# Performance work log

Measured on AMD Instinct MI355X. Metric: run time of the kernel, lower is better.

Reference implementation:

```python
import jax, jax.numpy as jnp
import numpy as np

C_IN, C_P1, C_G1, N_OUT = 512, 256, 256, 6
B, H, W = 256, 19, 19


def mish(x):
    return x * jnp.tanh(jax.nn.softplus(x))


def setup_inputs() -> dict:
    key = jax.random.key(0)
    ks = jax.random.split(key, 8)
    x = jax.random.normal(ks[0], (B, C_IN, H, W), dtype=jnp.float32)
    mask = jnp.ones((B, 1, H, W), dtype=jnp.float32)
    conv1p_w = jax.random.normal(ks[1], (C_P1, C_IN), dtype=jnp.float32) * (1.0 / np.sqrt(C_IN))
    conv1g_w = jax.random.normal(ks[2], (C_G1, C_IN), dtype=jnp.float32) * (1.0 / np.sqrt(C_IN))
    beta_g = jnp.zeros((C_G1,), dtype=jnp.float32)
    linear_g_w = jax.random.normal(ks[3], (C_P1, 3 * C_G1), dtype=jnp.float32) * (1.0 / np.sqrt(3 * C_G1))
    beta2 = jnp.zeros((C_P1,), dtype=jnp.float32)
    conv2p_w = jax.random.normal(ks[4], (N_OUT, C_P1), dtype=jnp.float32) * (0.3 / np.sqrt(C_P1))
    return {"x": x, "mask": mask, "conv1p_w": conv1p_w, "conv1g_w": conv1g_w,
            "beta_g": beta_g, "linear_g_w": linear_g_w, "beta2": beta2, "conv2p_w": conv2p_w}


def reference(x, mask, conv1p_w, conv1g_w, beta_g, linear_g_w, beta2, conv2p_w):
    # 1x1 convs are channel GEMMs
    outp = jnp.einsum('bchw,oc->bohw', x, conv1p_w)              # [B, C_P1, H, W]
    outg = jnp.einsum('bchw,oc->bohw', x, conv1g_w)              # [B, C_G1, H, W]
    # BiasMask (scale=None) + Mish
    outg = mish((outg + beta_g[None, :, None, None]) * mask)
    # KataGPool: mean, scaled mean, max (masked)
    mask_sum_hw = jnp.sum(mask, axis=(2, 3), keepdims=True)      # [B,1,1,1]
    layer_mean = jnp.sum(outg * mask, axis=(2, 3), keepdims=True) / mask_sum_hw
    layer_max = jnp.max(outg + (mask - 1.0), axis=(2, 3), keepdims=True)
    sqrt_off = (jnp.sqrt(mask_sum_hw) - 14.0) / 10.0
    pooled = jnp.concatenate([layer_mean, layer_mean * sqrt_off, layer_max], axis=1)  # [B, 3*C_G1, 1, 1]
    pooled = pooled[:, :, 0, 0]                                  # [B, 3*C_G1]
    g = pooled @ linear_g_w.T                                    # [B, C_P1]
    # broadcast-add, BiasMask, Mish
    outp = mish((outp + g[:, :, None, None] + beta2[None, :, None, None]) * mask)
    # final 1x1 conv + invalid-move penalty
    outp = jnp.einsum('bchw,oc->bohw', outp, conv2p_w)           # [B, 6, H, W]
    outp = outp - (1.0 - mask) * 5000.0
    return outp.reshape(outp.shape[0], outp.shape[1], -1)        # [B, 6, H*W]
```

## Files before the change

### kernel.cpp

```cpp
#include <hip/hip_runtime.h>
#include <math.h>

#define BATCH 256
#define CIN   512
#define CP    256
#define HW    361
#define NOUT  6

typedef short bf16x8 __attribute__((ext_vector_type(8)));
typedef float f32x4  __attribute__((ext_vector_type(4)));

__device__ __forceinline__ short f2bf(float f) {
    unsigned u = __float_as_uint(f);
    u += 0x7fffu + ((u >> 16) & 1u);
    return (short)(u >> 16);
}
__device__ __forceinline__ float bf2f(short s) {
    return __uint_as_float(((unsigned)(unsigned short)s) << 16);
}
__device__ __forceinline__ float mish_f(float v) {
    float u = __expf(v);
    float a = 1.f + u;
    float w = a * a;
    float r = v * (w - 1.f) * __builtin_amdgcn_rcpf(w + 1.f);
    return (v > 30.f) ? v : r;
}
__device__ __forceinline__ void gl_lds16(const void* g, void* l) {
    __builtin_amdgcn_global_load_lds(
        (const __attribute__((address_space(1))) void*)g,
        (__attribute__((address_space(3))) void*)l, 16, 0, 0);
}

__global__ __launch_bounds__(256) void k0_weights(
    const float* __restrict__ w1p, const float* __restrict__ w1g,
    short* __restrict__ wT)
{
    int g = blockIdx.x * 256 + threadIdx.x;
    int half = g >> 14;
    int kb   = (g >> 10) & 15;
    int row  = (g >> 2) & 255;
    int s    = g & 3;
    int sc   = s ^ ((row >> 1) & 3);
    const float* src = (half == 0) ? (w1p + (size_t)row * CIN)
                                   : (w1g + (size_t)row * CIN);
    int c = kb * 32 + sc * 8;
    float f[8];
    *(float4*)(f)     = *(const float4*)(src + c);
    *(float4*)(f + 4) = *(const float4*)(src + c + 4);
    bf16x8 v;
    #pragma unroll
    for (int i = 0; i < 8; ++i) v[i] = f2bf(f[i]);
    *(bf16x8*)((char*)wT + (size_t)half * 262144 + kb * 16384 + row * 64 + s * 16) = v;
}

__global__ __launch_bounds__(512, 4) void k1_conv1(
    const float* __restrict__ x, const short* __restrict__ wT,
    const float* __restrict__ mask, const float* __restrict__ beta_g,
    short* __restrict__ outp_pre, float* __restrict__ psum, float* __restrict__ pmax)
{
    int orig = blockIdx.x;
    int newid = (orig & 7) * 192 + (orig >> 3);
    int half = newid & 1;
    int nb = newid >> 1;
    int n = nb % 3;
    int b = nb / 3;

    const int tid = threadIdx.x;
    const int lane = tid & 63, wid = tid >> 6;
    const int wm = wid >> 1, wn = wid & 1;
    const int lc = lane & 15, lg = lane >> 4;
    const int hw0 = n * 128;

    __shared__ __align__(16) short As[3][8192];
    __shared__ __align__(16) short Bs[3][4096];
    __shared__ float maskS[128], betaS[256];
    float* redS = (float*)(&As[0][0]);
    float* redM = redS + 512;

    if (tid < 128) {
        int hwg_ = hw0 + tid;
        maskS[tid] = (hwg_ < HW) ? mask[b * HW + hwg_] : 0.f;
    }
    if (tid < 256) betaS[tid] = beta_g[tid];
    asm volatile("s_waitcnt vmcnt(0) lgkmcnt(0)" ::: "memory");
    __builtin_amdgcn_sched_barrier(0);

    const int brow = tid & 127;
    const int bs   = tid >> 7;
    const int hwg  = hw0 + brow;
    const bool bvalid = hwg < HW;
    const float* xb = x + ((size_t)b * CIN + bs * 8) * HW + hwg;
    const int bDstOff = brow * 64 + ((bs ^ ((brow >> 1) & 3)) * 16);
    char* bDstBase = (char*)Bs;

    const char* aSrc = (const char*)wT + (size_t)half * 262144 + tid * 16;
    char* aDst = (char*)As + tid * 16;

    int aOff[4], bOff[4];
    #pragma unroll
    for (int mf = 0; mf < 4; ++mf) {
        int r = wm * 64 + mf * 16 + lc;
        aOff[mf] = r * 64 + ((lg ^ ((r >> 1) & 3)) * 16);
    }
    #pragma unroll
    for (int nf = 0; nf < 4; ++nf) {
        int r = wn * 64 + nf * 16 + lc;
        bOff[nf] = r * 64 + ((lg ^ ((r >> 1) & 3)) * 16);
    }

    float regB[8];
    #pragma unroll
    for (int i = 0; i < 8; ++i) regB[i] = 0.f;

    f32x4 acc[4][4];
    #pragma unroll
    for (int i = 0; i < 4; ++i)
        #pragma unroll
        for (int j = 0; j < 4; ++j)
            acc[i][j] = (f32x4){0.f, 0.f, 0.f, 0.f};

#define BLOAD(kb)                                                          \
    do {                                                                   \
        const float* src_ = xb + (size_t)(kb) * 32 * HW;                   \
        _Pragma("unroll")                                                  \
        for (int i_ = 0; i_ < 8; ++i_) {                                   \
            regB[i_] = bvalid ? src_[(size_t)i_ * HW] : 0.f;               \
        }                                                                  \
    } while (0)

#define BWRITE(buf)                                                        \
    do {                                                                   \
        bf16x8 o_;                                                         \
        _Pragma("unroll")                                                  \
        for (int i_ = 0; i_ < 8; ++i_) o_[i_] = f2bf(regB[i_]);            \
        *(bf16x8*)(bDstBase + (buf) * 8192 + bDstOff) = o_;                \
    } while (0)

#define ALOAD(buf, kb)                                                     \
    do {                                                                   \
        gl_lds16(aSrc + (kb) * 16384,        aDst + (buf) * 16384);        \
        gl_lds16(aSrc + (kb) * 16384 + 8192, aDst + (buf) * 16384 + 8192); \
    } while (0)

    ALOAD(0, 0); BLOAD(0);
    ALOAD(1, 1);
    asm volatile("s_waitcnt vmcnt(2)" ::: "memory");
    __builtin_amdgcn_sched_barrier(0);
    BWRITE(0);
    BLOAD(1);
    asm volatile("s_waitcnt lgkmcnt(0)" ::: "memory");
    __builtin_amdgcn_s_barrier();
    __builtin_amdgcn_sched_barrier(0);

    #pragma unroll
    for (int t = 0; t < 16; ++t) {
        const int buf = t % 3;
        const char* ab = (const char*)As + buf * 16384;
        const char* bb = (const char*)Bs + buf * 8192;

        bf16x8 aF[4], bF[4];
        #pragma unroll
        for (int mf = 0; mf < 4; ++mf) aF[mf] = *(const bf16x8*)(ab + aOff[mf]);
        #pragma unroll
        for (int nf = 0; nf < 4; ++nf) bF[nf] = *(const bf16x8*)(bb + bOff[nf]);

        if (t < 14) { ALOAD((t + 2) % 3, t + 2); }

        __builtin_amdgcn_s_setprio(1);
        #pragma unroll
        for (int mf = 0; mf < 4; ++mf)
            #pragma unroll
            for (int nf = 0; nf < 4; ++nf)
                acc[mf][nf] = __builtin_amdgcn_mfma_f32_16x16x32_bf16(
                    aF[mf], bF[nf], acc[mf][nf], 0, 0, 0);
        __builtin_amdgcn_s_setprio(0);

        if (t < 14) {
            asm volatile("s_waitcnt vmcnt(2)" ::: "memory");
            __builtin_amdgcn_sched_barrier(0);
            BWRITE((t + 1) % 3);
            BLOAD(t + 2);
        } else if (t == 14) {
            asm volatile("s_waitcnt vmcnt(0)" ::: "memory");
            __builtin_amdgcn_sched_barrier(0);
            BWRITE(15 % 3);
        }
        if (t < 15) {
            asm volatile("s_waitcnt lgkmcnt(0)" ::: "memory");
            __builtin_amdgcn_s_barrier();
            __builtin_amdgcn_sched_barrier(0);
        }
    }
    __syncthreads();

    if (half == 0) {
        #pragma unroll
        for (int mf = 0; mf < 4; ++mf) {
            int ch = wm * 64 + mf * 16 + lg * 4;
            #pragma unroll
            for (int nf = 0; nf < 4; ++nf) {
                int hw = hw0 + wn * 64 + nf * 16 + lc;
                if (hw < HW) {
                    #pragma unroll
                    for (int j = 0; j < 4; ++j)
                        outp_pre[((size_t)(b * CP + ch + j)) * HW + hw] = f2bf(acc[mf][nf][j]);
                }
            }
        }
    } else {
        #pragma unroll
        for (int mf = 0; mf < 4; ++mf) {
            #pragma unroll
            for (int j = 0; j < 4; ++j) {
                int rloc = wm * 64 + mf * 16 + lg * 4 + j;
                float beta = betaS[rloc];
                float s = 0.f, mx = -INFINITY;
                #pragma unroll
                for (int nf = 0; nf < 4; ++nf) {
                    int cl = wn * 64 + nf * 16 + lc;
                    int hw = hw0 + cl;
                    float mv = maskS[cl];
                    float val = mish_f((acc[mf][nf][j] + beta) * mv);
                    if (hw < HW) {
                        s += val * mv;
                        mx = fmaxf(mx, val + mv - 1.f);
                    }
                }
                #pragma unroll
                for (int off = 1; off < 16; off <<= 1) {
                    s += __shfl_xor(s, off, 64);
                    mx = fmaxf(mx, __shfl_xor(mx, off, 64));
                }
                if (lc == 0) { redS[rloc * 2 + wn] = s; redM[rloc * 2 + wn] = mx; }
            }
        }
        __syncthreads();
        if (tid < 256) {
            float s = redS[tid * 2] + redS[tid * 2 + 1];
            float mx = fmaxf(redM[tid * 2], redM[tid * 2 + 1]);
            psum[((size_t)(b * CP + tid)) * 3 + n] = s;
            pmax[((size_t)(b * CP + tid)) * 3 + n] = mx;
        }
    }
#undef BLOAD
#undef BWRITE
#undef ALOAD
}

__global__ __launch_bounds__(256) void k2_pool_linear(
    const float* __restrict__ mask, const float* __restrict__ psum,
    const float* __restrict__ pmax, const float* __restrict__ lw,
    float* __restrict__ g_out)
{
    int b = blockIdx.x, t = threadIdx.x;
    __shared__ float pooled[768];
    __shared__ float msr[4];

    float s = 0.f;
    for (int i = t; i < HW; i += 256) s += mask[b * HW + i];
    #pragma unroll
    for (int off = 1; off < 64; off <<= 1) s += __shfl_xor(s, off, 64);
    if ((t & 63) == 0) msr[t >> 6] = s;
    __syncthreads();
    float msum = msr[0] + msr[1] + msr[2] + msr[3];

    {
        int c = t;
        const float* ps = psum + (size_t)(b * CP + c) * 3;
        const float* pm = pmax + (size_t)(b * CP + c) * 3;
        float s3 = ps[0] + ps[1] + ps[2];
        float m3 = fmaxf(fmaxf(pm[0], pm[1]), pm[2]);
        float mean = s3 / msum;
        float sq = (sqrtf(msum) - 14.f) * 0.1f;
        pooled[c] = mean; pooled[256 + c] = mean * sq; pooled[512 + c] = m3;
    }
    __syncthreads();
    {
        int o = t;
        const float4* wrow = (const float4*)(lw + (size_t)o * 768);
        float acc = 0.f;
        #pragma unroll 8
        for (int j = 0; j < 192; ++j) {
            float4 w4 = wrow[j];
            float4 p4 = *(const float4*)&pooled[j * 4];
            acc += p4.x * w4.x + p4.y * w4.y + p4.z * w4.z + p4.w * w4.w;
        }
        g_out[b * CP + o] = acc;
    }
}

__global__ __launch_bounds__(256) void k3_final(
    const short* __restrict__ outp_pre, const float* __restrict__ mask,
    const float* __restrict__ g_out, const float* __restrict__ beta2,
    const float* __restrict__ w2, float* __restrict__ out)
{
    int ht = blockIdx.x, b = blockIdx.y;
    int t = threadIdx.x;
    __shared__ float w2S[NOUT * 256];
    __shared__ float gbS[256];
    __shared__ float part[NOUT][256];

    for (int i = t; i < NOUT * 256; i += 256) w2S[i] = w2[i];
    gbS[t] = g_out[b * CP + t] + beta2[t];
    __syncthreads();

    int hw = t & 63, cg = t >> 6;
    int hwg = ht * 64 + hw;
    bool valid = hwg < HW;
    float maskv = valid ? mask[b * HW + hwg] : 0.f;

    float acc[NOUT] = {0.f, 0.f, 0.f, 0.f, 0.f, 0.f};
    const short* src = outp_pre + ((size_t)(b * CP + cg * 64)) * HW + hwg;
    #pragma unroll 4
    for (int ci = 0; ci < 64; ++ci) {
        float v = valid ? bf2f(src[(size_t)ci * HW]) : 0.f;
        float mm = mish_f((v + gbS[cg * 64 + ci]) * maskv);
        #pragma unroll
        for (int o = 0; o < NOUT; ++o) acc[o] += mm * w2S[o * 256 + cg * 64 + ci];
    }
    #pragma unroll
    for (int o = 0; o < NOUT; ++o) part[o][t] = acc[o];
    __syncthreads();

    for (int idx = t; idx < NOUT * 64; idx += 256) {
        int o = idx >> 6, h2 = idx & 63;
        int hg = ht * 64 + h2;
        if (hg < HW) {
            float mv = mask[b * HW + hg];
            float sum = part[o][h2] + part[o][64 + h2] + part[o][128 + h2] + part[o][192 + h2];
            out[((size_t)(b * NOUT + o)) * HW + hg] = sum - (1.f - mv) * 5000.f;
        }
    }
}

extern "C" void kernel_launch(void* const* d_in, const int* in_sizes, int n_in,
                              void* d_out, int out_size, void* d_ws, size_t ws_size,
                              hipStream_t stream) {
    const float* x     = (const float*)d_in[0];
    const float* mask  = (const float*)d_in[1];
    const float* w1p   = (const float*)d_in[2];
    const float* w1g   = (const float*)d_in[3];
    const float* betag = (const float*)d_in[4];
    const float* lw    = (const float*)d_in[5];
    const float* beta2 = (const float*)d_in[6];
    const float* w2    = (const float*)d_in[7];
    float* out = (float*)d_out;

    char* ws = (char*)d_ws;
    short* outp_pre = (short*)(ws);
    short* wT       = (short*)(ws + 47316992);
    float* psum     = (float*)(ws + 47841280);
    float* pmax     = (float*)(ws + 48627712);
    float* g_out    = (float*)(ws + 49414144);

    hipLaunchKernelGGL(k0_weights, dim3(128), dim3(256), 0, stream, w1p, w1g, wT);
    hipLaunchKernelGGL(k1_conv1, dim3(1536), dim3(512), 0, stream,
                       x, wT, mask, betag, outp_pre, psum, pmax);
    hipLaunchKernelGGL(k2_pool_linear, dim3(BATCH), dim3(256), 0, stream,
                       mask, psum, pmax, lw, g_out);
    hipLaunchKernelGGL(k3_final, dim3(6, BATCH), dim3(256), 0, stream,
                       outp_pre, mask, g_out, beta2, w2, out);
    (void)in_sizes; (void)n_in; (void)out_size; (void)ws_size;
}
```

Measured before the change: 142.9 us.

## Restructure conv1 tiles: full 512-channel M per block, whole-K x tile in LDS

Each block now computes all 512 output channels (both conv branches) for 64 spatial positions instead of one 256-channel half for 128 positions. The x tile for the block's full K extent is kept resident in LDS, so each x element is read from global memory once per block rather than once per half. The weight tile is no longer staged through LDS; MFMA A-fragments load directly from the global (cached) transposed weights. This drops the triple-buffered pipeline and most barriers, but puts weight fetches on the MFMA critical path, uses 64 KB of LDS per block, and doubles the number of pooling partials that k2 must reduce.

After: 161.2 us. +12.8%, slower.

```diff
diff --git a/kernel.cpp b/kernel.cpp
--- a/kernel.cpp
+++ b/kernel.cpp
@@ -6,6 +6,7 @@
 #define CP    256
 #define HW    361
 #define NOUT  6
+#define NT    6
 
 typedef short bf16x8 __attribute__((ext_vector_type(8)));
 typedef float f32x4  __attribute__((ext_vector_type(4)));
@@ -25,32 +26,25 @@
     float r = v * (w - 1.f) * __builtin_amdgcn_rcpf(w + 1.f);
     return (v > 30.f) ? v : r;
 }
-__device__ __forceinline__ void gl_lds16(const void* g, void* l) {
-    __builtin_amdgcn_global_load_lds(
-        (const __attribute__((address_space(1))) void*)g,
-        (__attribute__((address_space(3))) void*)l, 16, 0, 0);
-}
 
 __global__ __launch_bounds__(256) void k0_weights(
     const float* __restrict__ w1p, const float* __restrict__ w1g,
     short* __restrict__ wT)
 {
     int g = blockIdx.x * 256 + threadIdx.x;
-    int half = g >> 14;
-    int kb   = (g >> 10) & 15;
-    int row  = (g >> 2) & 255;
-    int s    = g & 3;
-    int sc   = s ^ ((row >> 1) & 3);
-    const float* src = (half == 0) ? (w1p + (size_t)row * CIN)
-                                   : (w1g + (size_t)row * CIN);
-    int c = kb * 32 + sc * 8;
+    int kb  = g >> 11;
+    int row = (g >> 2) & 511;
+    int s   = g & 3;
+    const float* src = (row < 256) ? (w1p + (size_t)row * CIN)
+                                   : (w1g + (size_t)(row - 256) * CIN);
+    int c = kb * 32 + s * 8;
     float f[8];
     *(float4*)(f)     = *(const float4*)(src + c);
     *(float4*)(f + 4) = *(const float4*)(src + c + 4);
     bf16x8 v;
     #pragma unroll
     for (int i = 0; i < 8; ++i) v[i] = f2bf(f[i]);
-    *(bf16x8*)((char*)wT + (size_t)half * 262144 + kb * 16384 + row * 64 + s * 16) = v;
+    *(bf16x8*)((char*)wT + (size_t)kb * 32768 + row * 64 + s * 16) = v;
 }
 
 __global__ __launch_bounds__(512, 4) void k1_conv1(
@@ -60,57 +54,55 @@
 {
     int orig = blockIdx.x;
     int newid = (orig & 7) * 192 + (orig >> 3);
-    int half = newid & 1;
-    int nb = newid >> 1;
-    int n = nb % 3;
-    int b = nb / 3;
+    int n = newid % NT;
+    int b = newid / NT;
 
     const int tid = threadIdx.x;
     const int lane = tid & 63, wid = tid >> 6;
-    const int wm = wid >> 1, wn = wid & 1;
     const int lc = lane & 15, lg = lane >> 4;
-    const int hw0 = n * 128;
-
-    __shared__ __align__(16) short As[3][8192];
-    __shared__ __align__(16) short Bs[3][4096];
-    __shared__ float maskS[128], betaS[256];
-    float* redS = (float*)(&As[0][0]);
-    float* redM = redS + 512;
-
-    if (tid < 128) {
+    const int hw0 = n * 64;
+
+    __shared__ __align__(16) short Bs[64 * 512];
+    __shared__ float maskS[64];
+    __shared__ float betaS[256];
+
+    if (tid < 64) {
         int hwg_ = hw0 + tid;
         maskS[tid] = (hwg_ < HW) ? mask[b * HW + hwg_] : 0.f;
     }
     if (tid < 256) betaS[tid] = beta_g[tid];
-    asm volatile("s_waitcnt vmcnt(0) lgkmcnt(0)" ::: "memory");
-    __builtin_amdgcn_sched_barrier(0);
-
-    const int brow = tid & 127;
-    const int bs   = tid >> 7;
+
+    const int brow = tid & 63;
+    const int bgrp = tid >> 6;
     const int hwg  = hw0 + brow;
     const bool bvalid = hwg < HW;
-    const float* xb = x + ((size_t)b * CIN + bs * 8) * HW + hwg;
-    const int bDstOff = brow * 64 + ((bs ^ ((brow >> 1) & 3)) * 16);
-    char* bDstBase = (char*)Bs;
-
-    const char* aSrc = (const char*)wT + (size_t)half * 262144 + tid * 16;
-    char* aDst = (char*)As + tid * 16;
-
-    int aOff[4], bOff[4];
-    #pragma unroll
-    for (int mf = 0; mf < 4; ++mf) {
-        int r = wm * 64 + mf * 16 + lc;
-        aOff[mf] = r * 64 + ((lg ^ ((r >> 1) & 3)) * 16);
-    }
+    const float* xb = x + (size_t)b * CIN * HW + hwg;
+
+#define BFILL(s_)                                                           \
+    do {                                                                    \
+        int s__ = (s_);                                                     \
+        const float* fsrc_ = xb + (size_t)(s__ * 8) * HW;                   \
+        bf16x8 o_;                                                          \
+        _Pragma("unroll")                                                   \
+        for (int i_ = 0; i_ < 8; ++i_)                                      \
+            o_[i_] = f2bf(bvalid ? fsrc_[(size_t)i_ * HW] : 0.f);           \
+        *(bf16x8*)((char*)Bs + brow * 1024 + ((s__ ^ (brow & 7)) * 16)) = o_; \
+    } while (0)
+
+    BFILL(bgrp);
+    BFILL(bgrp + 8);
+    BFILL(bgrp + 16);
+    BFILL(bgrp + 24);
+    __syncthreads();
+
+    const size_t aBase = (size_t)(wid * 64 + lc) * 64 + lg * 16;
+    const char* wTb = (const char*)wT;
+    int bRowOff[4];
     #pragma unroll
     for (int nf = 0; nf < 4; ++nf) {
-        int r = wn * 64 + nf * 16 + lc;
-        bOff[nf] = r * 64 + ((lg ^ ((r >> 1) & 3)) * 16);
-    }
-
-    float regB[8];
-    #pragma unroll
-    for (int i = 0; i < 8; ++i) regB[i] = 0.f;
+        int r = nf * 16 + lc;
+        bRowOff[nf] = r * 1024 + ((r & 7) * 16);
+    }
 
     f32x4 acc[4][4];
     #pragma unroll
@@ -119,87 +111,54 @@
         for (int j = 0; j < 4; ++j)
             acc[i][j] = (f32x4){0.f, 0.f, 0.f, 0.f};
 
-#define BLOAD(kb)                                                          \
-    do {                                                                   \
-        const float* src_ = xb + (size_t)(kb) * 32 * HW;                   \
-        _Pragma("unroll")                                                  \
-        for (int i_ = 0; i_ < 8; ++i_) {                                   \
-            regB[i_] = bvalid ? src_[(size_t)i_ * HW] : 0.f;               \
-        }                                                                  \
+#define KSTEP(ks_)                                                          \
+    do {                                                                    \
+        int ks__ = (ks_);                                                   \
+        const char* ap_ = wTb + (size_t)ks__ * 32768 + aBase;               \
+        bf16x8 aF[4], bF[4];                                                \
+        _Pragma("unroll")                                                   \
+        for (int mf_ = 0; mf_ < 4; ++mf_)                                   \
+            aF[mf_] = *(const bf16x8*)(ap_ + mf_ * 1024);                   \
+        _Pragma("unroll")                                                   \
+        for (int nf_ = 0; nf_ < 4; ++nf_)                                   \
+            bF[nf_] = *(const bf16x8*)((const char*)Bs +                    \
+                        (bRowOff[nf_] ^ ((ks__ * 4 + lg) * 16)));           \
+        _Pragma("unroll")                                                   \
+        for (int mf_ = 0; mf_ < 4; ++mf_)                                   \
+            _Pragma("unroll")                                               \
+            for (int nf_ = 0; nf_ < 4; ++nf_)                               \
+                acc[mf_][nf_] = __builtin_amdgcn_mfma_f32_16x16x32_bf16(    \
+                    aF[mf_], bF[nf_], acc[mf_][nf_], 0, 0, 0);              \
     } while (0)
 
-#define BWRITE(buf)                                                        \
-    do {                                                                   \
-        bf16x8 o_;                                                         \
-        _Pragma("unroll")                                                  \
-        for (int i_ = 0; i_ < 8; ++i_) o_[i_] = f2bf(regB[i_]);            \
-        *(bf16x8*)(bDstBase + (buf) * 8192 + bDstOff) = o_;                \
-    } while (0)
-
-#define ALOAD(buf, kb)                                                     \
-    do {                                                                   \
-        gl_lds16(aSrc + (kb) * 16384,        aDst + (buf) * 16384);        \
-        gl_lds16(aSrc + (kb) * 16384 + 8192, aDst + (buf) * 16384 + 8192); \
-    } while (0)
-
-    ALOAD(0, 0); BLOAD(0);
-    ALOAD(1, 1);
-    asm volatile("s_waitcnt vmcnt(2)" ::: "memory");
-    __builtin_amdgcn_sched_barrier(0);
-    BWRITE(0);
-    BLOAD(1);
-    asm volatile("s_waitcnt lgkmcnt(0)" ::: "memory");
-    __builtin_amdgcn_s_barrier();
-    __builtin_amdgcn_sched_barrier(0);
-
-    #pragma unroll
-    for (int t = 0; t < 16; ++t) {
-        const int buf = t % 3;
-        const char* ab = (const char*)As + buf * 16384;
-        const char* bb = (const char*)Bs + buf * 8192;
-
-        bf16x8 aF[4], bF[4];
-        #pragma unroll
-        for (int mf = 0; mf < 4; ++mf) aF[mf] = *(const bf16x8*)(ab + aOff[mf]);
-        #pragma unroll
-        for (int nf = 0; nf < 4; ++nf) bF[nf] = *(const bf16x8*)(bb + bOff[nf]);
-
-        if (t < 14) { ALOAD((t + 2) % 3, t + 2); }
-
-        __builtin_amdgcn_s_setprio(1);
-        #pragma unroll
-        for (int mf = 0; mf < 4; ++mf)
+    #pragma unroll
+    for (int kp = 0; kp < 4; ++kp) {
+        int sfill = 32 + kp * 8 + bgrp;
+        const float* fsrc = xb + (size_t)(sfill * 8) * HW;
+        float fr[8];
+        #pragma unroll
+        for (int i = 0; i < 8; ++i) fr[i] = bvalid ? fsrc[(size_t)i * HW] : 0.f;
+        KSTEP(kp * 2);
+        {
+            bf16x8 o;
             #pragma unroll
-            for (int nf = 0; nf < 4; ++nf)
-                acc[mf][nf] = __builtin_amdgcn_mfma_f32_16x16x32_bf16(
-                    aF[mf], bF[nf], acc[mf][nf], 0, 0, 0);
-        __builtin_amdgcn_s_setprio(0);
-
-        if (t < 14) {
-            asm volatile("s_waitcnt vmcnt(2)" ::: "memory");
-            __builtin_amdgcn_sched_barrier(0);
-            BWRITE((t + 1) % 3);
-            BLOAD(t + 2);
-        } else if (t == 14) {
-            asm volatile("s_waitcnt vmcnt(0)" ::: "memory");
-            __builtin_amdgcn_sched_barrier(0);
-            BWRITE(15 % 3);
-        }
-        if (t < 15) {
-            asm volatile("s_waitcnt lgkmcnt(0)" ::: "memory");
-            __builtin_amdgcn_s_barrier();
-            __builtin_amdgcn_sched_barrier(0);
-        }
-    }
-    __syncthreads();
-
-    if (half == 0) {
+            for (int i = 0; i < 8; ++i) o[i] = f2bf(fr[i]);
+            *(bf16x8*)((char*)Bs + brow * 1024 + ((sfill ^ (brow & 7)) * 16)) = o;
+        }
+        KSTEP(kp * 2 + 1);
+    }
+    __syncthreads();
+
+    #pragma unroll
+    for (int ks = 8; ks < 16; ++ks) KSTEP(ks);
+
+    if (wid < 4) {
         #pragma unroll
         for (int mf = 0; mf < 4; ++mf) {
-            int ch = wm * 64 + mf * 16 + lg * 4;
+            int ch = wid * 64 + mf * 16 + lg * 4;
             #pragma unroll
             for (int nf = 0; nf < 4; ++nf) {
-                int hw = hw0 + wn * 64 + nf * 16 + lc;
+                int hw = hw0 + nf * 16 + lc;
                 if (hw < HW) {
                     #pragma unroll
                     for (int j = 0; j < 4; ++j)
@@ -212,12 +171,12 @@
         for (int mf = 0; mf < 4; ++mf) {
             #pragma unroll
             for (int j = 0; j < 4; ++j) {
-                int rloc = wm * 64 + mf * 16 + lg * 4 + j;
+                int rloc = (wid - 4) * 64 + mf * 16 + lg * 4 + j;
                 float beta = betaS[rloc];
                 float s = 0.f, mx = -INFINITY;
                 #pragma unroll
                 for (int nf = 0; nf < 4; ++nf) {
-                    int cl = wn * 64 + nf * 16 + lc;
+                    int cl = nf * 16 + lc;
                     int hw = hw0 + cl;
                     float mv = maskS[cl];
                     float val = mish_f((acc[mf][nf][j] + beta) * mv);
@@ -231,20 +190,15 @@
                     s += __shfl_xor(s, off, 64);
                     mx = fmaxf(mx, __shfl_xor(mx, off, 64));
                 }
-                if (lc == 0) { redS[rloc * 2 + wn] = s; redM[rloc * 2 + wn] = mx; }
+                if (lc == 0) {
+                    psum[((size_t)(b * CP + rloc)) * NT + n] = s;
+                    pmax[((size_t)(b * CP + rloc)) * NT + n] = mx;
+                }
             }
         }
-        __syncthreads();
-        if (tid < 256) {
-            float s = redS[tid * 2] + redS[tid * 2 + 1];
-            float mx = fmaxf(redM[tid * 2], redM[tid * 2 + 1]);
-            psum[((size_t)(b * CP + tid)) * 3 + n] = s;
-            pmax[((size_t)(b * CP + tid)) * 3 + n] = mx;
-        }
-    }
-#undef BLOAD
-#undef BWRITE
-#undef ALOAD
+    }
+#undef BFILL
+#undef KSTEP
 }
 
 __global__ __launch_bounds__(256) void k2_pool_linear(
@@ -266,10 +220,11 @@
 
     {
         int c = t;
-        const float* ps = psum + (size_t)(b * CP + c) * 3;
-        const float* pm = pmax + (size_t)(b * CP + c) * 3;
-        float s3 = ps[0] + ps[1] + ps[2];
-        float m3 = fmaxf(fmaxf(pm[0], pm[1]), pm[2]);
+        const float* ps = psum + (size_t)(b * CP + c) * NT;
+        const float* pm = pmax + (size_t)(b * CP + c) * NT;
+        float s3 = 0.f, m3 = -INFINITY;
+        #pragma unroll
+        for (int i = 0; i < NT; ++i) { s3 += ps[i]; m3 = fmaxf(m3, pm[i]); }
         float mean = s3 / msum;
         float sq = (sqrtf(msum) - 14.f) * 0.1f;
         pooled[c] = mean; pooled[256 + c] = mean * sq; pooled[512 + c] = m3;
@@ -350,8 +305,8 @@
     short* outp_pre = (short*)(ws);
     short* wT       = (short*)(ws + 47316992);
     float* psum     = (float*)(ws + 47841280);
-    float* pmax     = (float*)(ws + 48627712);
-    float* g_out    = (float*)(ws + 49414144);
+    float* pmax     = (float*)(ws + 49414144);
+    float* g_out    = (float*)(ws + 50987008);
 
     hipLaunchKernelGGL(k0_weights, dim3(128), dim3(256), 0, stream, w1p, w1g, wT);
     hipLaunchKernelGGL(k1_conv1, dim3(1536), dim3(512), 0, stream,
```

## Retile conv1 so each block computes both weight halves over a 64-column spatial tile

Applied to the files above, without the earlier changes.

The conv1 kernel now computes all 512 output channels (conv1p and conv1g together) for a 64-wide spatial tile per block, instead of splitting the channel halves across blocks over 128-wide tiles. Each x tile is now loaded once for both GEMMs rather than twice. The weight prep is re-laid out so all 512 rows are interleaved per k-block, and the pipeline drops from triple to double buffering with a full wait every iteration. Each warp writes pooling partials directly to six per-tile slots, which removes the cross-warp LDS reduction, and the pool kernel sums six partials. In exchange, each block loads twice as much A data per step, only half the threads issue B loads, and the stricter vmcnt(0) wait each iteration may expose load latency.

Result: no change. 145.5 us (+1.8%).

```diff
diff --git a/kernel.cpp b/kernel.cpp
--- a/kernel.cpp
+++ b/kernel.cpp
@@ -6,6 +6,7 @@
 #define CP    256
 #define HW    361
 #define NOUT  6
+#define NT    6
 
 typedef short bf16x8 __attribute__((ext_vector_type(8)));
 typedef float f32x4  __attribute__((ext_vector_type(4)));
@@ -36,13 +37,12 @@
     short* __restrict__ wT)
 {
     int g = blockIdx.x * 256 + threadIdx.x;
-    int half = g >> 14;
-    int kb   = (g >> 10) & 15;
-    int row  = (g >> 2) & 255;
-    int s    = g & 3;
-    int sc   = s ^ ((row >> 1) & 3);
-    const float* src = (half == 0) ? (w1p + (size_t)row * CIN)
-                                   : (w1g + (size_t)row * CIN);
+    int kb  = g >> 11;
+    int row = (g >> 2) & 511;
+    int s   = g & 3;
+    int sc  = s ^ ((row >> 1) & 3);
+    const float* src = (row < 256) ? (w1p + (size_t)row * CIN)
+                                   : (w1g + (size_t)(row - 256) * CIN);
     int c = kb * 32 + sc * 8;
     float f[8];
     *(float4*)(f)     = *(const float4*)(src + c);
@@ -50,7 +50,7 @@
     bf16x8 v;
     #pragma unroll
     for (int i = 0; i < 8; ++i) v[i] = f2bf(f[i]);
-    *(bf16x8*)((char*)wT + (size_t)half * 262144 + kb * 16384 + row * 64 + s * 16) = v;
+    *(bf16x8*)((char*)wT + (size_t)kb * 32768 + row * 64 + s * 16) = v;
 }
 
 __global__ __launch_bounds__(512, 4) void k1_conv1(
@@ -60,24 +60,20 @@
 {
     int orig = blockIdx.x;
     int newid = (orig & 7) * 192 + (orig >> 3);
-    int half = newid & 1;
-    int nb = newid >> 1;
-    int n = nb % 3;
-    int b = nb / 3;
+    int n = newid % NT;
+    int b = newid / NT;
 
     const int tid = threadIdx.x;
     const int lane = tid & 63, wid = tid >> 6;
-    const int wm = wid >> 1, wn = wid & 1;
     const int lc = lane & 15, lg = lane >> 4;
-    const int hw0 = n * 128;
-
-    __shared__ __align__(16) short As[3][8192];
-    __shared__ __align__(16) short Bs[3][4096];
-    __shared__ float maskS[128], betaS[256];
-    float* redS = (float*)(&As[0][0]);
-    float* redM = redS + 512;
-
-    if (tid < 128) {
+    const int hw0 = n * 64;
+
+    __shared__ __align__(16) short As[2][16384];
+    __shared__ __align__(16) short Bs[2][2048];
+    __shared__ float maskS[64];
+    __shared__ float betaS[256];
+
+    if (tid < 64) {
         int hwg_ = hw0 + tid;
         maskS[tid] = (hwg_ < HW) ? mask[b * HW + hwg_] : 0.f;
     }
@@ -85,26 +81,27 @@
     asm volatile("s_waitcnt vmcnt(0) lgkmcnt(0)" ::: "memory");
     __builtin_amdgcn_sched_barrier(0);
 
-    const int brow = tid & 127;
-    const int bs   = tid >> 7;
+    const bool bduty = tid < 256;
+    const int brow = tid & 63;
+    const int bs   = (tid >> 6) & 3;
     const int hwg  = hw0 + brow;
-    const bool bvalid = hwg < HW;
+    const bool bvalid = bduty && (hwg < HW);
     const float* xb = x + ((size_t)b * CIN + bs * 8) * HW + hwg;
     const int bDstOff = brow * 64 + ((bs ^ ((brow >> 1) & 3)) * 16);
     char* bDstBase = (char*)Bs;
 
-    const char* aSrc = (const char*)wT + (size_t)half * 262144 + tid * 16;
+    const char* aSrc = (const char*)wT + tid * 16;
     char* aDst = (char*)As + tid * 16;
 
     int aOff[4], bOff[4];
     #pragma unroll
     for (int mf = 0; mf < 4; ++mf) {
-        int r = wm * 64 + mf * 16 + lc;
+        int r = wid * 64 + mf * 16 + lc;
         aOff[mf] = r * 64 + ((lg ^ ((r >> 1) & 3)) * 16);
     }
     #pragma unroll
     for (int nf = 0; nf < 4; ++nf) {
-        int r = wn * 64 + nf * 16 + lc;
+        int r = nf * 16 + lc;
         bOff[nf] = r * 64 + ((lg ^ ((r >> 1) & 3)) * 16);
     }
 
@@ -121,42 +118,45 @@
 
 #define BLOAD(kb)                                                          \
     do {                                                                   \
-        const float* src_ = xb + (size_t)(kb) * 32 * HW;                   \
-        _Pragma("unroll")                                                  \
-        for (int i_ = 0; i_ < 8; ++i_) {                                   \
-            regB[i_] = bvalid ? src_[(size_t)i_ * HW] : 0.f;               \
+        if (bduty) {                                                       \
+            const float* src_ = xb + (size_t)(kb) * 32 * HW;               \
+            _Pragma("unroll")                                              \
+            for (int i_ = 0; i_ < 8; ++i_)                                 \
+                regB[i_] = bvalid ? src_[(size_t)i_ * HW] : 0.f;           \
         }                                                                  \
     } while (0)
 
 #define BWRITE(buf)                                                        \
     do {                                                                   \
-        bf16x8 o_;                                                         \
-        _Pragma("unroll")                                                  \
-        for (int i_ = 0; i_ < 8; ++i_) o_[i_] = f2bf(regB[i_]);            \
-        *(bf16x8*)(bDstBase + (buf) * 8192 + bDstOff) = o_;                \
+        if (bduty) {                                                       \
+            bf16x8 o_;                                                     \
+            _Pragma("unroll")                                              \
+            for (int i_ = 0; i_ < 8; ++i_) o_[i_] = f2bf(regB[i_]);        \
+            *(bf16x8*)(bDstBase + (buf) * 4096 + bDstOff) = o_;            \
+        }                                                                  \
     } while (0)
 
 #define ALOAD(buf, kb)                                                     \
     do {                                                                   \
-        gl_lds16(aSrc + (kb) * 16384,        aDst + (buf) * 16384);        \
-        gl_lds16(aSrc + (kb) * 16384 + 8192, aDst + (buf) * 16384 + 8192); \
+        _Pragma("unroll")                                                  \
+        for (int l_ = 0; l_ < 4; ++l_)                                     \
+            gl_lds16(aSrc + (size_t)(kb) * 32768 + l_ * 8192,              \
+                     aDst + (buf) * 32768 + l_ * 8192);                    \
     } while (0)
 
-    ALOAD(0, 0); BLOAD(0);
-    ALOAD(1, 1);
-    asm volatile("s_waitcnt vmcnt(2)" ::: "memory");
+    BLOAD(0);
+    ALOAD(0, 0);
+    asm volatile("s_waitcnt vmcnt(4)" ::: "memory");
     __builtin_amdgcn_sched_barrier(0);
     BWRITE(0);
-    BLOAD(1);
-    asm volatile("s_waitcnt lgkmcnt(0)" ::: "memory");
+    asm volatile("s_waitcnt vmcnt(0) lgkmcnt(0)" ::: "memory");
     __builtin_amdgcn_s_barrier();
     __builtin_amdgcn_sched_barrier(0);
 
     #pragma unroll
     for (int t = 0; t < 16; ++t) {
-        const int buf = t % 3;
-        const char* ab = (const char*)As + buf * 16384;
-        const char* bb = (const char*)Bs + buf * 8192;
+        const char* ab = (const char*)As + (t & 1) * 32768;
+        const char* bb = (const char*)Bs + (t & 1) * 4096;
 
         bf16x8 aF[4], bF[4];
         #pragma unroll
@@ -164,7 +164,10 @@
         #pragma unroll
         for (int nf = 0; nf < 4; ++nf) bF[nf] = *(const bf16x8*)(bb + bOff[nf]);
 
-        if (t < 14) { ALOAD((t + 2) % 3, t + 2); }
+        if (t < 15) {
+            BLOAD(t + 1);
+            ALOAD((t + 1) & 1, t + 1);
+        }
 
         __builtin_amdgcn_s_setprio(1);
         #pragma unroll
@@ -175,31 +178,23 @@
                     aF[mf], bF[nf], acc[mf][nf], 0, 0, 0);
         __builtin_amdgcn_s_setprio(0);
 
-        if (t < 14) {
-            asm volatile("s_waitcnt vmcnt(2)" ::: "memory");
+        if (t < 15) {
+            asm volatile("s_waitcnt vmcnt(4)" ::: "memory");
             __builtin_amdgcn_sched_barrier(0);
-            BWRITE((t + 1) % 3);
-            BLOAD(t + 2);
-        } else if (t == 14) {
-            asm volatile("s_waitcnt vmcnt(0)" ::: "memory");
-            __builtin_amdgcn_sched_barrier(0);
-            BWRITE(15 % 3);
-        }
-        if (t < 15) {
-            asm volatile("s_waitcnt lgkmcnt(0)" ::: "memory");
+            BWRITE((t + 1) & 1);
+            asm volatile("s_waitcnt vmcnt(0) lgkmcnt(0)" ::: "memory");
             __builtin_amdgcn_s_barrier();
             __builtin_amdgcn_sched_barrier(0);
         }
     }
-    __syncthreads();
-
-    if (half == 0) {
+
+    if (wid < 4) {
         #pragma unroll
         for (int mf = 0; mf < 4; ++mf) {
-            int ch = wm * 64 + mf * 16 + lg * 4;
+            int ch = wid * 64 + mf * 16 + lg * 4;
             #pragma unroll
             for (int nf = 0; nf < 4; ++nf) {
-                int hw = hw0 + wn * 64 + nf * 16 + lc;
+                int hw = hw0 + nf * 16 + lc;
                 if (hw < HW) {
                     #pragma unroll
                     for (int j = 0; j < 4; ++j)
@@ -212,12 +207,12 @@
         for (int mf = 0; mf < 4; ++mf) {
             #pragma unroll
             for (int j = 0; j < 4; ++j) {
-                int rloc = wm * 64 + mf * 16 + lg * 4 + j;
+                int rloc = (wid - 4) * 64 + mf * 16 + lg * 4 + j;
                 float beta = betaS[rloc];
                 float s = 0.f, mx = -INFINITY;
                 #pragma unroll
                 for (int nf = 0; nf < 4; ++nf) {
-                    int cl = wn * 64 + nf * 16 + lc;
+                    int cl = nf * 16 + lc;
                     int hw = hw0 + cl;
                     float mv = maskS[cl];
                     float val = mish_f((acc[mf][nf][j] + beta) * mv);
@@ -231,15 +226,11 @@
                     s += __shfl_xor(s, off, 64);
                     mx = fmaxf(mx, __shfl_xor(mx, off, 64));
                 }
-                if (lc == 0) { redS[rloc * 2 + wn] = s; redM[rloc * 2 + wn] = mx; }
+                if (lc == 0) {
+                    psum[((size_t)(b * CP + rloc)) * NT + n] = s;
+                    pmax[((size_t)(b * CP + rloc)) * NT + n] = mx;
+                }
             }
-        }
-        __syncthreads();
-        if (tid < 256) {
-            float s = redS[tid * 2] + redS[tid * 2 + 1];
-            float mx = fmaxf(redM[tid * 2], redM[tid * 2 + 1]);
-            psum[((size_t)(b * CP + tid)) * 3 + n] = s;
-            pmax[((size_t)(b * CP + tid)) * 3 + n] = mx;
         }
     }
 #undef BLOAD
@@ -266,10 +257,11 @@
 
     {
         int c = t;
-        const float* ps = psum + (size_t)(b * CP + c) * 3;
-        const float* pm = pmax + (size_t)(b * CP + c) * 3;
-        float s3 = ps[0] + ps[1] + ps[2];
-        float m3 = fmaxf(fmaxf(pm[0], pm[1]), pm[2]);
+        const float* ps = psum + (size_t)(b * CP + c) * NT;
+        const float* pm = pmax + (size_t)(b * CP + c) * NT;
+        float s3 = 0.f, m3 = -INFINITY;
+        #pragma unroll
+        for (int i = 0; i < NT; ++i) { s3 += ps[i]; m3 = fmaxf(m3, pm[i]); }
         float mean = s3 / msum;
         float sq = (sqrtf(msum) - 14.f) * 0.1f;
         pooled[c] = mean; pooled[256 + c] = mean * sq; pooled[512 + c] = m3;
@@ -350,8 +342,8 @@
     short* outp_pre = (short*)(ws);
     short* wT       = (short*)(ws + 47316992);
     float* psum     = (float*)(ws + 47841280);
-    float* pmax     = (float*)(ws + 48627712);
-    float* g_out    = (float*)(ws + 49414144);
+    float* pmax     = (float*)(ws + 49414144);
+    float* g_out    = (float*)(ws + 50987008);
 
     hipLaunchKernelGGL(k0_weights, dim3(128), dim3(256), 0, stream, w1p, w1g, wT);
     hipLaunchKernelGGL(k1_conv1, dim3(1536), dim3(512), 0, stream,
```
